# Kernel optimization log

Hardware: AMD Instinct MI355X
Metric: run time of the kernel (lower is better)

The kernel has to match this reference:

```python
import jax, jax.numpy as jnp
import numpy as np

EPS = 1e-5
NUM_GROUPS = 32
NUM_HEADS = 8

def group_norm(x, w, b):
    # x: (B, C, H, W), 32 groups, affine per-channel
    B, C, H, W = x.shape
    xg = x.reshape(B, NUM_GROUPS, C // NUM_GROUPS, H, W)
    mu = xg.mean(axis=(2, 3, 4), keepdims=True)
    var = xg.var(axis=(2, 3, 4), keepdims=True)
    xn = ((xg - mu) * jax.lax.rsqrt(var + EPS)).reshape(B, C, H, W)
    return xn * w[None, :, None, None] + b[None, :, None, None]

def conv1x1(x, w, b):
    # 1x1 conv == per-pixel linear; w: (out, in), x: (B, C, H, W)
    return jnp.einsum('oc,bchw->bohw', w, x) + b[None, :, None, None]

def setup_inputs() -> dict:
    key = jax.random.key(0)
    ks = jax.random.split(key, 4)
    B, C, H, W = 2, 512, 64, 64
    s = 1.0 / np.sqrt(C)
    return {
        'x': jax.random.normal(ks[0], (B, C, H, W), jnp.float32),
        'gn_w': jnp.ones((C,), jnp.float32),
        'gn_b': jnp.zeros((C,), jnp.float32),
        'wq': jax.random.normal(ks[1], (C, C), jnp.float32) * s,
        'bq': jnp.zeros((C,), jnp.float32),
        'wkv': jax.random.normal(ks[2], (2 * C, C), jnp.float32) * s,
        'bkv': jnp.zeros((2 * C,), jnp.float32),
        'wo': jax.random.normal(ks[3], (C, C), jnp.float32) * s,
        'bo': jnp.zeros((C,), jnp.float32),
    }

def reference(x, gn_w, gn_b, wq, bq, wkv, bkv, wo, bo):
    B, C, H, W = x.shape
    hd = C // NUM_HEADS  # head_dim
    residual = x
    x_norm = group_norm(x, gn_w, gn_b)
    q = conv1x1(x_norm, wq, bq).reshape(B, NUM_HEADS, hd, H * W)
    kv = conv1x1(x_norm, wkv, bkv)
    k, v = jnp.split(kv, 2, axis=1)
    k = k.reshape(B, NUM_HEADS, hd, H * W)
    v = v.reshape(B, NUM_HEADS, hd, H * W)
    scale = hd ** (-0.5)
    attn = jnp.einsum('bhdi,bhdj->bhij', q, k) * scale
    attn = jax.nn.softmax(attn, axis=-1)
    out = jnp.einsum('bhij,bhdj->bhdi', attn, v).reshape(B, C, H, W)
    out = conv1x1(out, wo, bo)
    return out + residual
```

## Files before the change

kernel.cpp:

```cpp
#include <hip/hip_runtime.h>
#include <cmath>

typedef __bf16 bf16x8 __attribute__((ext_vector_type(8)));
typedef __bf16 bf16x4 __attribute__((ext_vector_type(4)));
typedef float  f32x4  __attribute__((ext_vector_type(4)));
typedef unsigned uint2_ev __attribute__((ext_vector_type(2)));

static __device__ __forceinline__ f32x4 mfma16(bf16x8 a, bf16x8 b, f32x4 c) {
    return __builtin_amdgcn_mfma_f32_16x16x32_bf16(a, b, c, 0, 0, 0);
}

static __device__ __forceinline__ float fast_exp2(float x) {
#if __has_builtin(__builtin_amdgcn_exp2f)
    return __builtin_amdgcn_exp2f(x);
#else
    return exp2f(x);
#endif
}

static __device__ __forceinline__ void quad_swap(unsigned &a, unsigned &b) {
#if __has_builtin(__builtin_amdgcn_permlane32_swap) && __has_builtin(__builtin_amdgcn_permlane16_swap)
    uint2_ev r32 = __builtin_amdgcn_permlane32_swap(a, b, false, false);
    uint2_ev r16 = __builtin_amdgcn_permlane16_swap(r32[0], r32[1], false, false);
    a = r16[0]; b = r16[1];
#else
    asm volatile("v_permlane32_swap_b32 %0, %1\n\t"
                 "v_permlane16_swap_b32 %0, %1"
                 : "+v"(a), "+v"(b));
#endif
}

static __device__ __forceinline__ void gload_lds16(const void* g, void* l) {
    __builtin_amdgcn_global_load_lds((const __attribute__((address_space(1))) void*)g,
                                     (__attribute__((address_space(3))) void*)l, 16, 0, 0);
}

#define OFF_STATS 0
#define OFF_BEFF  1024
#define OFF_W     16384
#define OFF_XNT   (4u*1024*1024)
#define OFF_QKT   (OFF_XNT + 8u*1024*1024)
#define OFF_V     (OFF_QKT + 16u*1024*1024)
#define OFF_OP    (OFF_V + 8u*1024*1024)
#define CHUNK_O   4194304u
#define CHUNK_L   65536u

__global__ __launch_bounds__(256) void gn_fuse(const float* __restrict__ x,
                                               float* __restrict__ stats,
                                               __bf16* __restrict__ xT) {
    int p0 = blockIdx.x * 64, c0 = blockIdx.y * 64, b = blockIdx.z;
    int tid = threadIdx.x, lane = tid & 63, wave = tid >> 6;
    __shared__ float t[64][68];
    __shared__ float red[4][8];
    float acc_s[4] = {0.f,0.f,0.f,0.f}, acc_ss[4] = {0.f,0.f,0.f,0.f};
    const int rr = tid >> 4;
    const int p4 = (tid & 15) * 4;
    #pragma unroll
    for (int i = 0; i < 4; ++i) {
        int cc = rr + 16*i;
        float4 v = *(const float4*)&x[((size_t)(b*512 + c0 + cc) << 12) + p0 + p4];
        *(float4*)&t[cc][p4] = v;
        acc_s[i]  += v.x + v.y + v.z + v.w;
        acc_ss[i] += v.x*v.x + v.y*v.y + v.z*v.z + v.w*v.w;
    }
    #pragma unroll
    for (int g = 0; g < 4; ++g) {
        #pragma unroll
        for (int off = 1; off < 64; off <<= 1) {
            acc_s[g]  += __shfl_xor(acc_s[g],  off);
            acc_ss[g] += __shfl_xor(acc_ss[g], off);
        }
    }
    if (lane == 0) {
        #pragma unroll
        for (int g = 0; g < 4; ++g) { red[wave][g*2] = acc_s[g]; red[wave][g*2+1] = acc_ss[g]; }
    }
    __syncthreads();
    if (tid < 8) {
        float v0 = red[0][tid] + red[1][tid] + red[2][tid] + red[3][tid];
        int g = (b << 5) + (c0 >> 4) + (tid >> 1);
        atomicAdd(&stats[g*2 + (tid & 1)], v0);
    }
    const int ch = tid & 7;
    #pragma unroll
    for (int w = 0; w < 2; ++w) {
        int pp = (tid >> 3) + 32*w;
        __bf16 ob[8];
        #pragma unroll
        for (int e = 0; e < 8; ++e) ob[e] = (__bf16)t[ch*8 + e][pp];
        *(bf16x8*)&xT[((size_t)(b*4096 + p0 + pp) << 9) + c0 + ch*8] = *(bf16x8*)ob;
    }
}

__global__ __launch_bounds__(256) void prep_w(const float* __restrict__ wq,
                                              const float* __restrict__ wkv,
                                              const float* __restrict__ wo,
                                              const float* __restrict__ bq,
                                              const float* __restrict__ bkv,
                                              const float* __restrict__ stats,
                                              const float* __restrict__ gw,
                                              const float* __restrict__ gb,
                                              __bf16* __restrict__ wS,
                                              __bf16* __restrict__ wo_bf,
                                              float* __restrict__ beff) {
    const int b = blockIdx.y, bx = blockIdx.x;
    const int tid = threadIdx.x, lane = tid & 63, wave = tid >> 6;
    if (bx >= 48) {
        if (b) return;
        int r0 = (bx - 48) * 32;
        #pragma unroll
        for (int ps = 0; ps < 8; ++ps) {
            int row = r0 + ps*4 + wave;
            __bf16 obuf[8];
            #pragma unroll
            for (int e = 0; e < 8; ++e) obuf[e] = (__bf16)wo[(size_t)row*512 + lane*8 + e];
            *(bf16x8*)&wo_bf[(size_t)row*512 + lane*8] = *(bf16x8*)obuf;
        }
        return;
    }
    __shared__ float sS[512], sT[512];
    for (int c = tid; c < 512; c += 256) {
        int g = (b << 5) + (c >> 4);
        float mu   = stats[g*2] * (1.f/65536.f);
        float var  = stats[g*2+1] * (1.f/65536.f) - mu*mu;
        float rstd = rsqrtf(var + 1e-5f);
        float s = rstd * gw[c];
        sS[c] = s;
        sT[c] = gb[c] - mu * s;
    }
    __syncthreads();
    int r0 = bx * 32;
    #pragma unroll
    for (int ps = 0; ps < 8; ++ps) {
        int row = r0 + ps*4 + wave;
        const float* Wrow = (row < 512) ? (wq + (size_t)row*512) : (wkv + (size_t)(row-512)*512);
        float bias0 = (row < 512) ? bq[row] : bkv[row - 512];
        float bp = 0.f;
        __bf16 obuf[8];
        #pragma unroll
        for (int e = 0; e < 8; ++e) {
            int c = lane*8 + e;
            float wv_ = Wrow[c];
            obuf[e] = (__bf16)(wv_ * sS[c]);
            bp += wv_ * sT[c];
        }
        *(bf16x8*)&wS[((size_t)b*1536 + row)*512 + lane*8] = *(bf16x8*)obuf;
        #pragma unroll
        for (int off = 1; off < 64; off <<= 1) bp += __shfl_xor(bp, off);
        if (lane == 0) beff[b*1536 + row] = bias0 + bp;
    }
}

__global__ __launch_bounds__(256) void gemm128_kernel(
    const __bf16* __restrict__ A, const __bf16* __restrict__ B,
    const float* __restrict__ bias, int nsplit,
    float scale0, void* __restrict__ out,
    int N, int K, long long strideA, long long strideB, long long strideO, int biasStride) {
    const int bz = blockIdx.z;
    A += strideA * bz;
    B += strideB * bz;
    const float* bb = bias + (size_t)bz * biasStride;
    const int m0 = blockIdx.x * 128, n0 = blockIdx.y * 128;
    const int tid = threadIdx.x, lane = tid & 63, wave = tid >> 6;
    const int quad = lane >> 4, l16 = lane & 15;
    const int wm = (wave >> 1) * 64, wn = (wave & 1) * 64;

    __shared__ __attribute__((aligned(16))) __bf16 lds_a[128][40];
    __shared__ __attribute__((aligned(16))) __bf16 lds_b[128][40];

    f32x4 acc[4][4];
    #pragma unroll
    for (int mt = 0; mt < 4; ++mt)
        #pragma unroll
        for (int nt = 0; nt < 4; ++nt)
            #pragma unroll
            for (int r = 0; r < 4; ++r) acc[mt][nt][r] = 0.f;

    const int row_s = tid >> 2;
    const int kc    = (tid & 3) << 3;

    uint4 ra0, ra1, rb0, rb1;
    const __bf16* Abase = A + (size_t)(m0 + row_s) * K + kc;
    const __bf16* Bbase = B + (size_t)(n0 + row_s) * K + kc;
    ra0 = *(const uint4*)Abase;
    ra1 = *(const uint4*)(Abase + (size_t)64 * K);
    rb0 = *(const uint4*)Bbase;
    rb1 = *(const uint4*)(Bbase + (size_t)64 * K);

    for (int kt = 0; kt < K; kt += 32) {
        *(uint4*)&lds_a[row_s][kc]      = ra0;
        *(uint4*)&lds_a[row_s + 64][kc] = ra1;
        *(uint4*)&lds_b[row_s][kc]      = rb0;
        *(uint4*)&lds_b[row_s + 64][kc] = rb1;
        __syncthreads();
        if (kt + 32 < K) {
            ra0 = *(const uint4*)(Abase + kt + 32);
            ra1 = *(const uint4*)(Abase + kt + 32 + (size_t)64 * K);
            rb0 = *(const uint4*)(Bbase + kt + 32);
            rb1 = *(const uint4*)(Bbase + kt + 32 + (size_t)64 * K);
        }
        bf16x8 af[4], bfr[4];
        #pragma unroll
        for (int mt = 0; mt < 4; ++mt)
            af[mt] = *(const bf16x8*)&lds_a[wm + mt*16 + l16][quad*8];
        #pragma unroll
        for (int nt = 0; nt < 4; ++nt)
            bfr[nt] = *(const bf16x8*)&lds_b[wn + nt*16 + l16][quad*8];
        #pragma unroll
        for (int mt = 0; mt < 4; ++mt)
            #pragma unroll
            for (int nt = 0; nt < 4; ++nt)
                acc[mt][nt] = mfma16(af[mt], bfr[nt], acc[mt][nt]);
        __syncthreads();
    }

    #pragma unroll
    for (int mt = 0; mt < 4; ++mt) {
        const int mrow = m0 + wm + mt*16 + quad*4;
        #pragma unroll
        for (int nt = 0; nt < 4; ++nt) {
            const int ncol = n0 + wn + nt*16 + l16;
            #pragma unroll
            for (int r = 0; r < 4; ++r) {
                const int m = mrow + r;
                float val = acc[mt][nt][r] + bb[ncol];
                if (ncol < nsplit) val *= scale0;
                ((__bf16*)out)[(size_t)strideO * bz + (size_t)m * N + ncol] = (__bf16)val;
            }
        }
    }
}

template<int OUT_F32, int HAS_RES>
__global__ __launch_bounds__(256) void gemm64_kernel(
    const __bf16* __restrict__ A, const __bf16* __restrict__ B,
    const float* __restrict__ bias, const float* __restrict__ res,
    void* __restrict__ out,
    int N, int K, long long strideA, long long strideB, long long strideO, int biasStride) {
    const int bz = blockIdx.z;
    A += strideA * bz;
    B += strideB * bz;
    const float* bb = bias + (size_t)bz * biasStride;
    const int m0 = blockIdx.x * 64, n0 = blockIdx.y * 128;
    const int tid = threadIdx.x, lane = tid & 63, wave = tid >> 6;
    const int quad = lane >> 4, l16 = lane & 15;
    const int wn = wave * 32;

    __shared__ __attribute__((aligned(16))) __bf16 lds_a[64][40];
    __shared__ __attribute__((aligned(16))) __bf16 lds_b[128][40];

    f32x4 acc[4][2];
    #pragma unroll
    for (int mt = 0; mt < 4; ++mt)
        #pragma unroll
        for (int nt = 0; nt < 2; ++nt)
            #pragma unroll
            for (int r = 0; r < 4; ++r) acc[mt][nt][r] = 0.f;

    const int row_s = tid >> 2;
    const int kc    = (tid & 3) << 3;

    uint4 ra0, rb0, rb1;
    const __bf16* Abase = A + (size_t)(m0 + row_s) * K + kc;
    const __bf16* Bbase = B + (size_t)(n0 + row_s) * K + kc;
    ra0 = *(const uint4*)Abase;
    rb0 = *(const uint4*)Bbase;
    rb1 = *(const uint4*)(Bbase + (size_t)64 * K);

    for (int kt = 0; kt < K; kt += 32) {
        *(uint4*)&lds_a[row_s][kc]      = ra0;
        *(uint4*)&lds_b[row_s][kc]      = rb0;
        *(uint4*)&lds_b[row_s + 64][kc] = rb1;
        __syncthreads();
        if (kt + 32 < K) {
            ra0 = *(const uint4*)(Abase + kt + 32);
            rb0 = *(const uint4*)(Bbase + kt + 32);
            rb1 = *(const uint4*)(Bbase + kt + 32 + (size_t)64 * K);
        }
        bf16x8 af[4], bfr[2];
        #pragma unroll
        for (int mt = 0; mt < 4; ++mt)
            af[mt] = *(const bf16x8*)&lds_a[mt*16 + l16][quad*8];
        #pragma unroll
        for (int nt = 0; nt < 2; ++nt)
            bfr[nt] = *(const bf16x8*)&lds_b[wn + nt*16 + l16][quad*8];
        #pragma unroll
        for (int mt = 0; mt < 4; ++mt)
            #pragma unroll
            for (int nt = 0; nt < 2; ++nt)
                acc[mt][nt] = mfma16(af[mt], bfr[nt], acc[mt][nt]);
        __syncthreads();
    }

    #pragma unroll
    for (int mt = 0; mt < 4; ++mt) {
        const int mrow = m0 + mt*16 + quad*4;
        #pragma unroll
        for (int nt = 0; nt < 2; ++nt) {
            const int ncol = n0 + wn + nt*16 + l16;
            #pragma unroll
            for (int r = 0; r < 4; ++r) {
                const int m = mrow + r;
                float val = acc[mt][nt][r] + bb[m];
                const size_t idx = (size_t)strideO * bz + (size_t)m * N + ncol;
                if constexpr (HAS_RES) val += res[idx];
                if constexpr (OUT_F32) ((float*)out)[idx] = val;
                else ((__bf16*)out)[idx] = (__bf16)val;
            }
        }
    }
}

template<int NCH>
__global__ __launch_bounds__(256, 3) void attn_kernel(const __bf16* __restrict__ qkT,
                                                      const __bf16* __restrict__ v,
                                                      __bf16* __restrict__ attnT,
                                                      __bf16* __restrict__ Opart,
                                                      float* __restrict__ Lpart) {
    const int b = blockIdx.y >> 3, h = blockIdx.y & 7;
    const int chunk = (NCH > 1) ? blockIdx.z : 0;
    int NITER, kt0;
    if constexpr (NCH == 3) {
        NITER = (chunk == 0) ? 22 : 21;
        kt0   = (chunk == 0) ? 0 : (chunk == 1 ? 1408 : 2752);
    } else {
        NITER = 64 / NCH;
        kt0   = chunk * (4096 / NCH);
    }
    const int tid = threadIdx.x;
    const int wave = tid >> 6, lane = tid & 63;
    const int quad = lane >> 4, l16 = lane & 15;
    const int qbase = blockIdx.x * 256 + wave * 64;

    const __bf16* qkTb = qkT + ((size_t)b << 22);
    const __bf16* vb   = v   + ((size_t)b << 21);

    __shared__ __attribute__((aligned(16))) __bf16 lds_k[2][64][64];
    __shared__ __attribute__((aligned(16))) __bf16 lds_v[2][64][64];

    bf16x8 aq[4][2];
    #pragma unroll
    for (int mt = 0; mt < 4; ++mt) {
        const __bf16* qrow = qkTb + (size_t)(qbase + mt*16 + l16) * 1024 + h*64 + quad*8;
        aq[mt][0] = *(const bf16x8*)qrow;
        aq[mt][1] = *(const bf16x8*)(qrow + 32);
    }
    f32x4 o[4][5];
    #pragma unroll
    for (int mt = 0; mt < 4; ++mt)
        #pragma unroll
        for (int dt = 0; dt < 5; ++dt)
            #pragma unroll
            for (int r = 0; r < 4; ++r) o[mt][dt][r] = 0.f;
    const f32x4 kZero = {0.f, 0.f, 0.f, 0.f};

    bf16x8 onesb;
    #pragma unroll
    for (int e = 0; e < 8; ++e) onesb[e] = (__bf16)1.0f;

    const int myrow = (wave << 3) + (lane >> 3);
    const int mych  = ((lane & 7) ^ (myrow & 7)) << 3;
    const __bf16* kgb = qkTb + (size_t)myrow * 1024 + 512 + h*64 + mych;
    const __bf16* vgb = vb + ((size_t)(h*64 + myrow) << 12) + mych;

    auto stage = [&](int buf, int kt) {
        char* kb = (char*)(&lds_k[buf][0][0]) + (wave << 10);
        char* vp = (char*)(&lds_v[buf][0][0]) + (wave << 10);
        const __bf16* kg = kgb + (size_t)kt * 1024;
        const __bf16* vg = vgb + kt;
        gload_lds16(kg,                       kb);
        gload_lds16(kg + 32*1024,             kb + 4096);
        gload_lds16(vg,                       vp);
        gload_lds16(vg + ((size_t)32 << 12),  vp + 4096);
    };

    stage(0, kt0);

    for (int it = 0; it < NITER; ++it) {
        __syncthreads();
        const int cur = it & 1;
        if (it + 1 < NITER) stage(cur ^ 1, kt0 + (it + 1) * 64);

        #pragma unroll
        for (int kh = 0; kh < 2; ++kh) {
            __builtin_amdgcn_s_setprio(1);
            unsigned pd[4][4];
            #pragma unroll
            for (int j = 0; j < 2; ++j) {
                const int nt = kh*2 + j;
                const int kr = nt*16 + l16;
                bf16x8 bk0 = *(const bf16x8*)&lds_k[cur][kr][( quad      ^ (l16 & 7)) * 8];
                bf16x8 bk1 = *(const bf16x8*)&lds_k[cur][kr][((4 + quad) ^ (l16 & 7)) * 8];
                #pragma unroll
                for (int mt = 0; mt < 4; ++mt) {
                    f32x4 s = mfma16(bk1, aq[mt][1], mfma16(bk0, aq[mt][0], kZero));
                    f32x4 p;
                    #pragma unroll
                    for (int r = 0; r < 4; ++r) p[r] = fast_exp2(s[r]);
                    bf16x4 pb = __builtin_convertvector(p, bf16x4);
                    union { bf16x4 v; unsigned d[2]; } u; u.v = pb;
                    pd[mt][j*2]     = u.d[0];
                    pd[mt][j*2 + 1] = u.d[1];
                }
            }
            bf16x8 pa[4];
            #pragma unroll
            for (int mt = 0; mt < 4; ++mt) {
                unsigned x0 = pd[mt][0], x1 = pd[mt][1];
                unsigned y0 = pd[mt][2], y1 = pd[mt][3];
                quad_swap(x0, y0);
                quad_swap(x1, y1);
                union { unsigned d[4]; bf16x8 v; } u;
                u.d[0] = x0; u.d[1] = x1; u.d[2] = y0; u.d[3] = y1;
                pa[mt] = u.v;
            }
            #pragma unroll
            for (int dt = 0; dt < 4; ++dt) {
                bf16x8 bv = *(const bf16x8*)&lds_v[cur][dt*16 + l16][((kh*4 + quad) ^ (l16 & 7)) * 8];
                #pragma unroll
                for (int mt = 0; mt < 4; ++mt)
                    o[mt][dt] = mfma16(pa[mt], bv, o[mt][dt]);
            }
            #pragma unroll
            for (int mt = 0; mt < 4; ++mt)
                o[mt][4] = mfma16(pa[mt], onesb, o[mt][4]);
            __builtin_amdgcn_s_setprio(0);
        }
    }

    if constexpr (NCH > 1) {
        __bf16* Ob = Opart + (size_t)chunk * CHUNK_O;
        #pragma unroll
        for (int mt = 0; mt < 4; ++mt)
            #pragma unroll
            for (int dt = 0; dt < 4; ++dt)
                #pragma unroll
                for (int r = 0; r < 4; ++r) {
                    size_t row = (size_t)b * 4096 + qbase + mt*16 + quad*4 + r;
                    Ob[(row << 9) + (h << 6) + dt*16 + l16] = (__bf16)o[mt][dt][r];
                }
        if (l16 == 0) {
            #pragma unroll
            for (int mt = 0; mt < 4; ++mt)
                #pragma unroll
                for (int r = 0; r < 4; ++r) {
                    int p = qbase + mt*16 + quad*4 + r;
                    Lpart[(size_t)chunk * CHUNK_L + (size_t)(((b*8 + h)) << 12) + p] = o[mt][4][r];
                }
        }
    } else {
        #pragma unroll
        for (int mt = 0; mt < 4; ++mt) {
            float inv[4];
            #pragma unroll
            for (int r = 0; r < 4; ++r)
                inv[r] = 1.f / __shfl(o[mt][4][r], lane & 48);
            #pragma unroll
            for (int dt = 0; dt < 4; ++dt)
                #pragma unroll
                for (int r = 0; r < 4; ++r) {
                    size_t row = (size_t)b * 4096 + qbase + mt*16 + quad*4 + r;
                    attnT[(row << 9) + (h << 6) + dt*16 + l16] = (__bf16)(o[mt][dt][r] * inv[r]);
                }
        }
    }
}

template<int NCH>
__global__ __launch_bounds__(256) void attn_combine(const __bf16* __restrict__ Opart,
                                                    const float* __restrict__ Lpart,
                                                    __bf16* __restrict__ attnT) {
    int i = blockIdx.x * 256 + threadIdx.x;
    int c8 = i & 63;
    int p  = (i >> 6) & 4095;
    int b  = i >> 18;
    int h  = c8 >> 3;
    size_t lidx = (size_t)((b*8 + h) << 12) + p;
    float l = 0.f;
    #pragma unroll
    for (int ch = 0; ch < NCH; ++ch) l += Lpart[(size_t)ch * CHUNK_L + lidx];
    float inv = 1.f / l;
    size_t oi = ((size_t)(b*4096 + p) << 9) + c8*8;
    float acc[8] = {0.f,0.f,0.f,0.f,0.f,0.f,0.f,0.f};
    #pragma unroll
    for (int ch = 0; ch < NCH; ++ch) {
        bf16x8 ov = *(const bf16x8*)&Opart[(size_t)ch * CHUNK_O + oi];
        #pragma unroll
        for (int r = 0; r < 8; ++r) acc[r] += (float)ov[r];
    }
    bf16x8 rv;
    #pragma unroll
    for (int r = 0; r < 8; ++r) rv[r] = (__bf16)(acc[r] * inv);
    *(bf16x8*)&attnT[oi] = rv;
}

extern "C" void kernel_launch(void* const* d_in, const int* in_sizes, int n_in,
                              void* d_out, int out_size, void* d_ws, size_t ws_size,
                              hipStream_t stream) {
    const float* x   = (const float*)d_in[0];
    const float* gnw = (const float*)d_in[1];
    const float* gnb = (const float*)d_in[2];
    const float* wq  = (const float*)d_in[3];
    const float* bq  = (const float*)d_in[4];
    const float* wkv = (const float*)d_in[5];
    const float* bkv = (const float*)d_in[6];
    const float* wo  = (const float*)d_in[7];
    const float* bo  = (const float*)d_in[8];
    float* out = (float*)d_out;

    char* ws = (char*)d_ws;
    float*  stats  = (float*)(ws + OFF_STATS);
    float*  beff   = (float*)(ws + OFF_BEFF);
    __bf16* wS     = (__bf16*)(ws + OFF_W);
    __bf16* wo_bf  = wS + 2u*1536*512;
    __bf16* xT     = (__bf16*)(ws + OFF_XNT);
    __bf16* qkT    = (__bf16*)(ws + OFF_QKT);
    __bf16* vv     = (__bf16*)(ws + OFF_V);
    __bf16* Opart  = (__bf16*)(ws + OFF_OP);
    __bf16* attnT  = xT;

    const size_t need3 = (size_t)OFF_OP + 3u * (CHUNK_O * 2 + CHUNK_L * 4);
    const size_t need2 = (size_t)OFF_OP + 2u * (CHUNK_O * 2 + CHUNK_L * 4);
    const int nch = (ws_size >= need3) ? 3 : (ws_size >= need2 ? 2 : 1);
    float* Lpart = (float*)(ws + OFF_OP + (size_t)nch * CHUNK_O * 2);

    hipMemsetAsync(stats, 0, 512, stream);
    gn_fuse<<<dim3(64, 8, 2), 256, 0, stream>>>(x, stats, xT);
    prep_w<<<dim3(64, 2), 256, 0, stream>>>(wq, wkv, wo, bq, bkv, stats, gnw, gnb,
                                            wS, wo_bf, beff);

    const long long S  = 2097152LL;
    const long long S2 = 4194304LL;
    const long long SW = 1536LL*512;
    gemm128_kernel<<<dim3(32, 8, 2), 256, 0, stream>>>(
        xT, wS, beff, 512, 0.125f * 1.44269504f, qkT, 1024, 512, S, SW, S2, 1536);
    gemm64_kernel<0,0><<<dim3(8, 32, 2), 256, 0, stream>>>(
        wS + 1024*512, xT, beff + 1024, nullptr, vv, 4096, 512, SW, S, S, 1536);

    if (nch == 3) {
        attn_kernel<3><<<dim3(16, 16, 3), 256, 0, stream>>>(qkT, vv, nullptr, Opart, Lpart);
        attn_combine<3><<<2048, 256, 0, stream>>>(Opart, Lpart, attnT);
    } else if (nch == 2) {
        attn_kernel<2><<<dim3(16, 16, 2), 256, 0, stream>>>(qkT, vv, nullptr, Opart, Lpart);
        attn_combine<2><<<2048, 256, 0, stream>>>(Opart, Lpart, attnT);
    } else {
        attn_kernel<1><<<dim3(16, 16, 1), 256, 0, stream>>>(qkT, vv, attnT, nullptr, nullptr);
    }

    gemm64_kernel<1,1><<<dim3(8, 32, 2), 256, 0, stream>>>(
        wo_bf, attnT, bo, x, out, 4096, 512, 0, S, S, 0);
}
```

Measured before the change: 220.0 us.

## Use direct global-to-LDS double-buffered loads in GEMMs, drop 3-chunk attention split

Both GEMM kernels now stage tiles with global-to-LDS direct loads into double-buffered, XOR-swizzled shared memory with a 64-wide K step. This replaces the register-staged copy and one of the two barriers per iteration. The aim is to overlap the next tile's fetch with MFMA work and avoid LDS bank conflicts. The attention split-K path also drops the 3-chunk variant and falls back to at most 2 chunks, which changes how much parallelism the attention stage has.

```diff
diff --git a/kernel.cpp b/kernel.cpp
--- a/kernel.cpp
+++ b/kernel.cpp
@@ -165,8 +165,8 @@
     const int quad = lane >> 4, l16 = lane & 15;
     const int wm = (wave >> 1) * 64, wn = (wave & 1) * 64;
 
-    __shared__ __attribute__((aligned(16))) __bf16 lds_a[128][40];
-    __shared__ __attribute__((aligned(16))) __bf16 lds_b[128][40];
+    __shared__ __attribute__((aligned(16))) __bf16 lds_a[2][128][64];
+    __shared__ __attribute__((aligned(16))) __bf16 lds_b[2][128][64];
 
     f32x4 acc[4][4];
     #pragma unroll
@@ -176,42 +176,42 @@
             #pragma unroll
             for (int r = 0; r < 4; ++r) acc[mt][nt][r] = 0.f;
 
-    const int row_s = tid >> 2;
-    const int kc    = (tid & 3) << 3;
-
-    uint4 ra0, ra1, rb0, rb1;
-    const __bf16* Abase = A + (size_t)(m0 + row_s) * K + kc;
-    const __bf16* Bbase = B + (size_t)(n0 + row_s) * K + kc;
-    ra0 = *(const uint4*)Abase;
-    ra1 = *(const uint4*)(Abase + (size_t)64 * K);
-    rb0 = *(const uint4*)Bbase;
-    rb1 = *(const uint4*)(Bbase + (size_t)64 * K);
-
-    for (int kt = 0; kt < K; kt += 32) {
-        *(uint4*)&lds_a[row_s][kc]      = ra0;
-        *(uint4*)&lds_a[row_s + 64][kc] = ra1;
-        *(uint4*)&lds_b[row_s][kc]      = rb0;
-        *(uint4*)&lds_b[row_s + 64][kc] = rb1;
+    const int myrow = (wave << 3) + (lane >> 3);
+    const int mych  = ((lane & 7) ^ (myrow & 7)) << 3;
+    const __bf16* Ab = A + (size_t)(m0 + myrow) * K + mych;
+    const __bf16* Bb = B + (size_t)(n0 + myrow) * K + mych;
+
+    auto stage = [&](int buf, int kt) {
+        char* la = (char*)(&lds_a[buf][0][0]) + (wave << 10);
+        char* lb = (char*)(&lds_b[buf][0][0]) + (wave << 10);
+        #pragma unroll
+        for (int i = 0; i < 4; ++i) {
+            gload_lds16(Ab + kt + (size_t)(32*i) * K, la + i*4096);
+            gload_lds16(Bb + kt + (size_t)(32*i) * K, lb + i*4096);
+        }
+    };
+
+    stage(0, 0);
+    const int NK = K >> 6;
+    for (int k8 = 0; k8 < NK; ++k8) {
         __syncthreads();
-        if (kt + 32 < K) {
-            ra0 = *(const uint4*)(Abase + kt + 32);
-            ra1 = *(const uint4*)(Abase + kt + 32 + (size_t)64 * K);
-            rb0 = *(const uint4*)(Bbase + kt + 32);
-            rb1 = *(const uint4*)(Bbase + kt + 32 + (size_t)64 * K);
-        }
-        bf16x8 af[4], bfr[4];
-        #pragma unroll
-        for (int mt = 0; mt < 4; ++mt)
-            af[mt] = *(const bf16x8*)&lds_a[wm + mt*16 + l16][quad*8];
-        #pragma unroll
-        for (int nt = 0; nt < 4; ++nt)
-            bfr[nt] = *(const bf16x8*)&lds_b[wn + nt*16 + l16][quad*8];
-        #pragma unroll
-        for (int mt = 0; mt < 4; ++mt)
+        const int cur = k8 & 1;
+        if (k8 + 1 < NK) stage(cur ^ 1, (k8 + 1) << 6);
+        #pragma unroll
+        for (int kh = 0; kh < 2; ++kh) {
+            bf16x8 af[4], bfr[4];
+            #pragma unroll
+            for (int mt = 0; mt < 4; ++mt)
+                af[mt] = *(const bf16x8*)&lds_a[cur][wm + mt*16 + l16][(((kh<<2)|quad) ^ (l16 & 7)) * 8];
             #pragma unroll
             for (int nt = 0; nt < 4; ++nt)
-                acc[mt][nt] = mfma16(af[mt], bfr[nt], acc[mt][nt]);
-        __syncthreads();
+                bfr[nt] = *(const bf16x8*)&lds_b[cur][wn + nt*16 + l16][(((kh<<2)|quad) ^ (l16 & 7)) * 8];
+            #pragma unroll
+            for (int mt = 0; mt < 4; ++mt)
+                #pragma unroll
+                for (int nt = 0; nt < 4; ++nt)
+                    acc[mt][nt] = mfma16(af[mt], bfr[nt], acc[mt][nt]);
+        }
     }
 
     #pragma unroll
@@ -246,8 +246,8 @@
     const int quad = lane >> 4, l16 = lane & 15;
     const int wn = wave * 32;
 
-    __shared__ __attribute__((aligned(16))) __bf16 lds_a[64][40];
-    __shared__ __attribute__((aligned(16))) __bf16 lds_b[128][40];
+    __shared__ __attribute__((aligned(16))) __bf16 lds_a[2][64][64];
+    __shared__ __attribute__((aligned(16))) __bf16 lds_b[2][128][64];
 
     f32x4 acc[4][2];
     #pragma unroll
@@ -257,39 +257,43 @@
             #pragma unroll
             for (int r = 0; r < 4; ++r) acc[mt][nt][r] = 0.f;
 
-    const int row_s = tid >> 2;
-    const int kc    = (tid & 3) << 3;
-
-    uint4 ra0, rb0, rb1;
-    const __bf16* Abase = A + (size_t)(m0 + row_s) * K + kc;
-    const __bf16* Bbase = B + (size_t)(n0 + row_s) * K + kc;
-    ra0 = *(const uint4*)Abase;
-    rb0 = *(const uint4*)Bbase;
-    rb1 = *(const uint4*)(Bbase + (size_t)64 * K);
-
-    for (int kt = 0; kt < K; kt += 32) {
-        *(uint4*)&lds_a[row_s][kc]      = ra0;
-        *(uint4*)&lds_b[row_s][kc]      = rb0;
-        *(uint4*)&lds_b[row_s + 64][kc] = rb1;
+    const int myrow = (wave << 3) + (lane >> 3);
+    const int mych  = ((lane & 7) ^ (myrow & 7)) << 3;
+    const __bf16* Ab = A + (size_t)(m0 + myrow) * K + mych;
+    const __bf16* Bb = B + (size_t)(n0 + myrow) * K + mych;
+
+    auto stage = [&](int buf, int kt) {
+        char* la = (char*)(&lds_a[buf][0][0]) + (wave << 10);
+        char* lb = (char*)(&lds_b[buf][0][0]) + (wave << 10);
+        #pragma unroll
+        for (int i = 0; i < 2; ++i)
+            gload_lds16(Ab + kt + (size_t)(32*i) * K, la + i*4096);
+        #pragma unroll
+        for (int i = 0; i < 4; ++i)
+            gload_lds16(Bb + kt + (size_t)(32*i) * K, lb + i*4096);
+    };
+
+    stage(0, 0);
+    const int NK = K >> 6;
+    for (int k8 = 0; k8 < NK; ++k8) {
         __syncthreads();
-        if (kt + 32 < K) {
-            ra0 = *(const uint4*)(Abase + kt + 32);
-            rb0 = *(const uint4*)(Bbase + kt + 32);
-            rb1 = *(const uint4*)(Bbase + kt + 32 + (size_t)64 * K);
-        }
-        bf16x8 af[4], bfr[2];
-        #pragma unroll
-        for (int mt = 0; mt < 4; ++mt)
-            af[mt] = *(const bf16x8*)&lds_a[mt*16 + l16][quad*8];
-        #pragma unroll
-        for (int nt = 0; nt < 2; ++nt)
-            bfr[nt] = *(const bf16x8*)&lds_b[wn + nt*16 + l16][quad*8];
-        #pragma unroll
-        for (int mt = 0; mt < 4; ++mt)
+        const int cur = k8 & 1;
+        if (k8 + 1 < NK) stage(cur ^ 1, (k8 + 1) << 6);
+        #pragma unroll
+        for (int kh = 0; kh < 2; ++kh) {
+            bf16x8 af[4], bfr[2];
+            #pragma unroll
+            for (int mt = 0; mt < 4; ++mt)
+                af[mt] = *(const bf16x8*)&lds_a[cur][mt*16 + l16][(((kh<<2)|quad) ^ (l16 & 7)) * 8];
             #pragma unroll
             for (int nt = 0; nt < 2; ++nt)
-                acc[mt][nt] = mfma16(af[mt], bfr[nt], acc[mt][nt]);
-        __syncthreads();
+                bfr[nt] = *(const bf16x8*)&lds_b[cur][wn + nt*16 + l16][(((kh<<2)|quad) ^ (l16 & 7)) * 8];
+            #pragma unroll
+            for (int mt = 0; mt < 4; ++mt)
+                #pragma unroll
+                for (int nt = 0; nt < 2; ++nt)
+                    acc[mt][nt] = mfma16(af[mt], bfr[nt], acc[mt][nt]);
+        }
     }
 
     #pragma unroll
@@ -319,14 +323,8 @@
                                                       float* __restrict__ Lpart) {
     const int b = blockIdx.y >> 3, h = blockIdx.y & 7;
     const int chunk = (NCH > 1) ? blockIdx.z : 0;
-    int NITER, kt0;
-    if constexpr (NCH == 3) {
-        NITER = (chunk == 0) ? 22 : 21;
-        kt0   = (chunk == 0) ? 0 : (chunk == 1 ? 1408 : 2752);
-    } else {
-        NITER = 64 / NCH;
-        kt0   = chunk * (4096 / NCH);
-    }
+    const int NITER = 64 / NCH;
+    const int kt0 = chunk * (4096 / NCH);
     const int tid = threadIdx.x;
     const int wave = tid >> 6, lane = tid & 63;
     const int quad = lane >> 4, l16 = lane & 15;
@@ -519,9 +517,8 @@
     __bf16* Opart  = (__bf16*)(ws + OFF_OP);
     __bf16* attnT  = xT;
 
-    const size_t need3 = (size_t)OFF_OP + 3u * (CHUNK_O * 2 + CHUNK_L * 4);
     const size_t need2 = (size_t)OFF_OP + 2u * (CHUNK_O * 2 + CHUNK_L * 4);
-    const int nch = (ws_size >= need3) ? 3 : (ws_size >= need2 ? 2 : 1);
+    const int nch = (ws_size >= need2) ? 2 : 1;
     float* Lpart = (float*)(ws + OFF_OP + (size_t)nch * CHUNK_O * 2);
 
     hipMemsetAsync(stats, 0, 512, stream);
@@ -537,10 +534,7 @@
     gemm64_kernel<0,0><<<dim3(8, 32, 2), 256, 0, stream>>>(
         wS + 1024*512, xT, beff + 1024, nullptr, vv, 4096, 512, SW, S, S, 1536);
 
-    if (nch == 3) {
-        attn_kernel<3><<<dim3(16, 16, 3), 256, 0, stream>>>(qkT, vv, nullptr, Opart, Lpart);
-        attn_combine<3><<<2048, 256, 0, stream>>>(Opart, Lpart, attnT);
-    } else if (nch == 2) {
+    if (nch == 2) {
         attn_kernel<2><<<dim3(16, 16, 2), 256, 0, stream>>>(qkT, vv, nullptr, Opart, Lpart);
         attn_combine<2><<<2048, 256, 0, stream>>>(Opart, Lpart, attnT);
     } else {
```

New measurement: 214.7 us. -2.4%, faster.
